# Performance work log

Measured on AMD Instinct MI355X. Metric: run time of the kernel, lower is better.

## Reference

```python
import jax, jax.numpy as jnp
import numpy as np

EMBED_DIM = 1024
NUM_HEADS = 16
HEAD_DIM = EMBED_DIM // NUM_HEADS
SCALE = float(np.sqrt(HEAD_DIM))


def setup_inputs() -> dict:
    key = jax.random.key(0)
    ks = jax.random.split(key, 7)
    B, S, E = 2, 2048, EMBED_DIM
    query = jax.random.normal(ks[0], (B, S, E), dtype=jnp.float32)
    key_t = jax.random.normal(ks[1], (B, S, E), dtype=jnp.float32)
    value = jax.random.normal(ks[2], (B, S, E), dtype=jnp.float32)
    # nn.Linear(E, E, bias=False): weight shape (out, in); y = x @ W.T
    std = 1.0 / np.sqrt(E)
    Wq = jax.random.uniform(ks[3], (E, E), jnp.float32, -std, std)
    Wk = jax.random.uniform(ks[4], (E, E), jnp.float32, -std, std)
    Wv = jax.random.uniform(ks[5], (E, E), jnp.float32, -std, std)
    Wo = jax.random.uniform(ks[6], (E, E), jnp.float32, -std, std)
    return {"query": query, "key": key_t, "value": value,
            "Wq": Wq, "Wk": Wk, "Wv": Wv, "Wo": Wo}


def reference(query, key, value, Wq, Wk, Wv, Wo):
    B, S, E = query.shape
    H, D = NUM_HEADS, HEAD_DIM
    q = (query @ Wq.T).reshape(B, S, H, D).transpose(0, 2, 1, 3)  # [B,H,S,D]
    k = (key @ Wk.T).reshape(B, S, H, D).transpose(0, 2, 1, 3)
    v = (value @ Wv.T).reshape(B, S, H, D).transpose(0, 2, 1, 3)
    scores = jnp.einsum('bhqd,bhkd->bhqk', q, k) / SCALE  # [B,H,S,S]
    attn = jax.nn.softmax(scores, axis=-1)
    out = jnp.einsum('bhqk,bhkd->bhqd', attn, v)  # [B,H,S,D]
    out = out.transpose(0, 2, 1, 3).reshape(B, S, E)
    return out @ Wo.T
```

## Files before the change

kernel.cpp:

```cpp
#include <hip/hip_runtime.h>
#include <hip/hip_bf16.h>
#include <math.h>

typedef float f32x4 __attribute__((ext_vector_type(4)));
typedef __bf16 bf16x8 __attribute__((ext_vector_type(8)));
typedef unsigned short u16;
typedef u16 u16x8 __attribute__((ext_vector_type(8)));
typedef u16 u16x4 __attribute__((ext_vector_type(4)));

__device__ __forceinline__ u16 f2bf(float f) {
    unsigned u = __builtin_bit_cast(unsigned, f);
    u = (u + 0x7fffu + ((u >> 16) & 1u)) >> 16;
    return (u16)u;
}
__device__ __forceinline__ unsigned pack2_rhu(float a, float b) {
    return __builtin_amdgcn_perm(__builtin_bit_cast(unsigned, b) + 0x8000u,
                                 __builtin_bit_cast(unsigned, a) + 0x8000u,
                                 0x07060302u);
}

#if __has_builtin(__builtin_amdgcn_exp2f)
#define EXP2(x) __builtin_amdgcn_exp2f(x)
#else
#define EXP2(x) exp2f(x)
#endif

__device__ __forceinline__ void gload16(const u16* g, u16* l) {
    __builtin_amdgcn_global_load_lds(
        (const __attribute__((address_space(1))) unsigned int*)(g),
        (__attribute__((address_space(3))) unsigned int*)(l), 16, 0, 0);
}

__global__ __launch_bounds__(256) void cast_all(
    const float* __restrict__ q, const float* __restrict__ k, const float* __restrict__ v,
    const float* __restrict__ wq, const float* __restrict__ wk, const float* __restrict__ wv,
    const float* __restrict__ wo, u16* __restrict__ dst) {
    int i = blockIdx.x * 256 + threadIdx.x;
    const float* src;
    int off;
    if (i < 3145728) {
        int seg = i >> 20;
        src = (seg == 0) ? q : (seg == 1) ? k : v;
        off = i - (seg << 20);
    } else {
        int j = (i - 3145728) >> 18;
        src = (j == 0) ? wq : (j == 1) ? wk : (j == 2) ? wv : wo;
        off = (i - 3145728) - (j << 18);
    }
    float4 val = ((const float4*)src)[off];
    u16x4 o4;
    o4.x = f2bf(val.x); o4.y = f2bf(val.y); o4.z = f2bf(val.z); o4.w = f2bf(val.w);
    ((u16x4*)dst)[i] = o4;
}

__global__ __launch_bounds__(256) void qkv_gemm(
    const u16* __restrict__ Xq, const u16* __restrict__ Xk, const u16* __restrict__ Xv,
    const u16* __restrict__ Wq, const u16* __restrict__ Wk, const u16* __restrict__ Wv,
    u16* __restrict__ Qo, u16* __restrict__ Ko, u16* __restrict__ Vto) {
    constexpr int K = 1024;
    const int z = blockIdx.z;
    const u16* __restrict__ A = (z == 0) ? Xq : (z == 1) ? Xk : Xv;
    const u16* __restrict__ W = (z == 0) ? Wq : (z == 1) ? Wk : Wv;
    u16* __restrict__ Out = (z == 0) ? Qo : (z == 1) ? Ko : Vto;

    __shared__ __align__(16) u16 As[128 * 64];
    __shared__ __align__(16) u16 Bs[128 * 64];

    const int t = threadIdx.x;
    const int lane = t & 63, wave = t >> 6;
    const int quad = lane >> 4, c = lane & 15, cx = c & 7;
    const int wr = (wave >> 1) * 64, wc = (wave & 1) * 64;
    const int rowA0 = blockIdx.y * 128;
    const int colB0 = blockIdx.x * 128;

    const int l3 = lane >> 3, l7 = lane & 7;
    const int chs = (l7 ^ l3) << 3;
    const u16* gA[4];
    const u16* gB[4];
    u16* lA[4];
    u16* lB[4];
#pragma unroll
    for (int i = 0; i < 4; ++i) {
        int row = wave * 32 + i * 8 + l3;
        gA[i] = A + (size_t)(rowA0 + row) * K + chs;
        gB[i] = W + (size_t)(colB0 + row) * K + chs;
        lA[i] = As + (wave * 256 + i * 64) * 8;
        lB[i] = Bs + (wave * 256 + i * 64) * 8;
    }

    const f32x4 zero4 = {0.f, 0.f, 0.f, 0.f};
    f32x4 acc[4][4];
#pragma unroll
    for (int i = 0; i < 4; ++i)
#pragma unroll
        for (int j = 0; j < 4; ++j) acc[i][j] = zero4;

    for (int kt = 0; kt < K; kt += 64) {
        __syncthreads();
#pragma unroll
        for (int i = 0; i < 4; ++i) {
            gload16(gA[i] + kt, lA[i]);
            gload16(gB[i] + kt, lB[i]);
        }
        __syncthreads();
#pragma unroll
        for (int ks = 0; ks < 2; ++ks) {
            const int co = ((ks * 4 + quad) ^ cx) << 3;
            bf16x8 af[4], bfr[4];
#pragma unroll
            for (int i = 0; i < 4; ++i)
                af[i] = *(const bf16x8*)(As + (wr + i * 16 + c) * 64 + co);
#pragma unroll
            for (int j = 0; j < 4; ++j)
                bfr[j] = *(const bf16x8*)(Bs + (wc + j * 16 + c) * 64 + co);
            if (z == 2) {
#pragma unroll
                for (int i = 0; i < 4; ++i)
#pragma unroll
                    for (int j = 0; j < 4; ++j)
                        acc[i][j] = __builtin_amdgcn_mfma_f32_16x16x32_bf16(bfr[j], af[i], acc[i][j], 0, 0, 0);
            } else {
#pragma unroll
                for (int i = 0; i < 4; ++i)
#pragma unroll
                    for (int j = 0; j < 4; ++j)
                        acc[i][j] = __builtin_amdgcn_mfma_f32_16x16x32_bf16(af[i], bfr[j], acc[i][j], 0, 0, 0);
            }
        }
    }

    const float scale = (z == 0) ? 0.18033688011112042f : 1.0f;
#pragma unroll
    for (int i = 0; i < 4; ++i) {
#pragma unroll
        for (int j = 0; j < 4; ++j) {
#pragma unroll
            for (int r = 0; r < 4; ++r) {
                float v = acc[i][j][r];
                if (z == 2) {
                    int n = colB0 + wc + j * 16 + quad * 4 + r;
                    int m = rowA0 + wr + i * 16 + c;
                    int b = m >> 11, s = m & 2047, h = n >> 6, d = n & 63;
                    Out[((((b << 4) | h) << 6) + d) * 2048 + s] = f2bf(v);
                } else {
                    int m = rowA0 + wr + i * 16 + quad * 4 + r;
                    int n = colB0 + wc + j * 16 + c;
                    int b = m >> 11, s = m & 2047, h = n >> 6, d = n & 63;
                    Out[((((b << 4) | h) * 2048 + s) << 6) + d] = f2bf(v * scale);
                }
            }
        }
    }
}

__global__ __launch_bounds__(256, 2) void out_gemm(const u16* __restrict__ A,
                                                   const u16* __restrict__ W,
                                                   float* __restrict__ Out) {
    constexpr int K = 1024;
    __shared__ __align__(16) u16 As[64 * 64];
    __shared__ __align__(16) u16 Bs[128 * 64];
    const int t = threadIdx.x;
    const int lane = t & 63, wave = t >> 6;
    const int quad = lane >> 4, c = lane & 15, cx = c & 7;
    const int wr = (wave >> 1) * 32, wc = (wave & 1) * 64;
    const int rowA0 = blockIdx.y * 64;
    const int colB0 = blockIdx.x * 128;

    const int l3 = lane >> 3, l7 = lane & 7;
    const int chs = (l7 ^ l3) << 3;
    const u16* gA[2];
    const u16* gB[4];
    u16* lA[2];
    u16* lB[4];
#pragma unroll
    for (int i = 0; i < 2; ++i) {
        int row = wave * 16 + i * 8 + l3;
        gA[i] = A + (size_t)(rowA0 + row) * K + chs;
        lA[i] = As + (wave * 128 + i * 64) * 8;
    }
#pragma unroll
    for (int i = 0; i < 4; ++i) {
        int row = wave * 32 + i * 8 + l3;
        gB[i] = W + (size_t)(colB0 + row) * K + chs;
        lB[i] = Bs + (wave * 256 + i * 64) * 8;
    }

    const f32x4 zero4 = {0.f, 0.f, 0.f, 0.f};
    f32x4 acc[2][4];
#pragma unroll
    for (int i = 0; i < 2; ++i)
#pragma unroll
        for (int j = 0; j < 4; ++j) acc[i][j] = zero4;

    for (int kt = 0; kt < K; kt += 64) {
        __syncthreads();
#pragma unroll
        for (int i = 0; i < 2; ++i) gload16(gA[i] + kt, lA[i]);
#pragma unroll
        for (int i = 0; i < 4; ++i) gload16(gB[i] + kt, lB[i]);
        __syncthreads();
#pragma unroll
        for (int ks = 0; ks < 2; ++ks) {
            const int co = ((ks * 4 + quad) ^ cx) << 3;
            bf16x8 af[2], bfr[4];
#pragma unroll
            for (int i = 0; i < 2; ++i)
                af[i] = *(const bf16x8*)(As + (wr + i * 16 + c) * 64 + co);
#pragma unroll
            for (int j = 0; j < 4; ++j)
                bfr[j] = *(const bf16x8*)(Bs + (wc + j * 16 + c) * 64 + co);
#pragma unroll
            for (int i = 0; i < 2; ++i)
#pragma unroll
                for (int j = 0; j < 4; ++j)
                    acc[i][j] = __builtin_amdgcn_mfma_f32_16x16x32_bf16(af[i], bfr[j], acc[i][j], 0, 0, 0);
        }
    }
#pragma unroll
    for (int i = 0; i < 2; ++i)
#pragma unroll
        for (int j = 0; j < 4; ++j)
#pragma unroll
            for (int r = 0; r < 4; ++r) {
                int m = rowA0 + wr + i * 16 + quad * 4 + r;
                int n = colB0 + wc + j * 16 + c;
                Out[(m << 10) + n] = acc[i][j][r];
            }
}

__global__ __launch_bounds__(256, 2) void flash_attn(const u16* __restrict__ Qp,
                                                     const u16* __restrict__ Kp,
                                                     const u16* __restrict__ Vt,
                                                     u16* __restrict__ Ob) {
    constexpr int S = 2048;
    const int bh = blockIdx.y;
    const int b = bh >> 4, h = bh & 15;
    const int t = threadIdx.x, wave = t >> 6, lane = t & 63;
    const int quad = lane >> 4, c = lane & 15, cx = c & 7;
    const int qw = blockIdx.x * 128 + wave * 32;
    const u16* Qb = Qp + (bh * S + qw) * 64;
    const u16* Kb = Kp + (bh * S) * 64;
    const u16* Vb = Vt + bh * 64 * S;

    __shared__ __align__(16) u16 Ks[2][64 * 64];
    __shared__ __align__(16) u16 Vs[2][64 * 64];
    __shared__ __align__(16) u16 Ps[4][32 * 64];
    u16* Pw = &Ps[wave][0];

    bf16x8 qf[2][2];
#pragma unroll
    for (int qt = 0; qt < 2; ++qt)
#pragma unroll
        for (int hf = 0; hf < 2; ++hf)
            qf[qt][hf] = *(const bf16x8*)(Qb + (qt * 16 + c) * 64 + hf * 32 + quad * 8);

    const int l3 = lane >> 3, l7 = lane & 7;
    const int chs = (l7 ^ l3) << 3;
    const u16* gK[2];
    const u16* gV[2];
    int lbase[2];
#pragma unroll
    for (int i = 0; i < 2; ++i) {
        int row = wave * 16 + i * 8 + l3;
        gK[i] = Kb + row * 64 + chs;
        gV[i] = Vb + row * 2048 + chs;
        lbase[i] = (wave * 128 + i * 64) * 8;
    }
#pragma unroll
    for (int i = 0; i < 2; ++i) {
        gload16(gK[i], &Ks[0][lbase[i]]);
        gload16(gV[i], &Vs[0][lbase[i]]);
    }
    __syncthreads();

    const f32x4 zero4 = {0.f, 0.f, 0.f, 0.f};
    f32x4 o[2][4];
#pragma unroll
    for (int qt = 0; qt < 2; ++qt)
#pragma unroll
        for (int t2 = 0; t2 < 4; ++t2) o[qt][t2] = zero4;
    float lsum[2] = {0.f, 0.f};

    for (int it = 0; it < S / 64; ++it) {
        const int cur = it & 1;
        if (it + 1 < S / 64) {
#pragma unroll
            for (int i = 0; i < 2; ++i) {
                gload16(gK[i] + (it + 1) * 4096, &Ks[cur ^ 1][lbase[i]]);
                gload16(gV[i] + (it + 1) * 64, &Vs[cur ^ 1][lbase[i]]);
            }
        }
        const u16* Kc = &Ks[cur][0];
        const u16* Vc = &Vs[cur][0];
        const int co0 = (quad ^ cx) << 3, co1 = ((4 + quad) ^ cx) << 3;
        f32x4 sc[4][2];
#pragma unroll
        for (int kt = 0; kt < 4; ++kt) {
            const int krow = (kt * 16 + c) * 64;
            bf16x8 kf0 = *(const bf16x8*)(Kc + krow + co0);
            bf16x8 kf1 = *(const bf16x8*)(Kc + krow + co1);
#pragma unroll
            for (int qt = 0; qt < 2; ++qt) {
                f32x4 zz = zero4;
                zz = __builtin_amdgcn_mfma_f32_16x16x32_bf16(kf0, qf[qt][0], zz, 0, 0, 0);
                zz = __builtin_amdgcn_mfma_f32_16x16x32_bf16(kf1, qf[qt][1], zz, 0, 0, 0);
                sc[kt][qt] = zz;
            }
        }
#pragma unroll
        for (int kt = 0; kt < 4; ++kt) {
            const int pchunk = ((kt * 2 + (quad >> 1)) ^ cx) << 3;
#pragma unroll
            for (int qt = 0; qt < 2; ++qt) {
                float p0 = EXP2(sc[kt][qt][0]);
                float p1 = EXP2(sc[kt][qt][1]);
                float p2 = EXP2(sc[kt][qt][2]);
                float p3 = EXP2(sc[kt][qt][3]);
                lsum[qt] += (p0 + p1) + (p2 + p3);
                uint2 pk;
                pk.x = pack2_rhu(p0, p1);
                pk.y = pack2_rhu(p2, p3);
                *(uint2*)(Pw + (qt * 16 + c) * 64 + pchunk + (quad & 1) * 4) = pk;
            }
        }
        __asm__ __volatile__("s_waitcnt lgkmcnt(0)" ::: "memory");
        bf16x8 pf[2][2];
#pragma unroll
        for (int qt = 0; qt < 2; ++qt) {
            pf[qt][0] = *(const bf16x8*)(Pw + (qt * 16 + c) * 64 + co0);
            pf[qt][1] = *(const bf16x8*)(Pw + (qt * 16 + c) * 64 + co1);
        }
#pragma unroll
        for (int t2 = 0; t2 < 4; ++t2) {
            const int vrow = (t2 * 16 + c) * 64;
            bf16x8 vf0 = *(const bf16x8*)(Vc + vrow + co0);
            bf16x8 vf1 = *(const bf16x8*)(Vc + vrow + co1);
#pragma unroll
            for (int qt = 0; qt < 2; ++qt) {
                o[qt][t2] = __builtin_amdgcn_mfma_f32_16x16x32_bf16(pf[qt][0], vf0, o[qt][t2], 0, 0, 0);
                o[qt][t2] = __builtin_amdgcn_mfma_f32_16x16x32_bf16(pf[qt][1], vf1, o[qt][t2], 0, 0, 0);
            }
        }
        __syncthreads();
    }
#pragma unroll
    for (int qt = 0; qt < 2; ++qt) {
        lsum[qt] += __shfl_xor(lsum[qt], 16);
        lsum[qt] += __shfl_xor(lsum[qt], 32);
    }
#pragma unroll
    for (int qt = 0; qt < 2; ++qt)
#pragma unroll
        for (int r = 0; r < 4; ++r) {
            float inv = 1.f / __shfl(lsum[qt], quad * 4 + r);
            int row = qw + qt * 16 + quad * 4 + r;
            int base = ((b * S + row) * 16 + h) * 64;
#pragma unroll
            for (int t2 = 0; t2 < 4; ++t2)
                Ob[base + t2 * 16 + c] = f2bf(o[qt][t2][r] * inv);
        }
}

extern "C" void kernel_launch(void* const* d_in, const int* in_sizes, int n_in,
                              void* d_out, int out_size, void* d_ws, size_t ws_size,
                              hipStream_t stream) {
    const float* q  = (const float*)d_in[0];
    const float* k  = (const float*)d_in[1];
    const float* v  = (const float*)d_in[2];
    const float* wq = (const float*)d_in[3];
    const float* wk = (const float*)d_in[4];
    const float* wv = (const float*)d_in[5];
    const float* wo = (const float*)d_in[6];

    u16* ws = (u16*)d_ws;
    u16* qb  = ws;
    u16* kb  = ws + 4194304;
    u16* vb  = ws + 8388608;
    u16* wqb = ws + 12582912;
    u16* wkb = ws + 13631488;
    u16* wvb = ws + 14680064;
    u16* wob = ws + 15728640;
    u16* Qp  = ws + 16777216;
    u16* Kp  = ws + 20971520;
    u16* Vtp = ws + 25165824;
    u16* Obf = ws + 29360128;

    cast_all<<<16384, 256, 0, stream>>>(q, k, v, wq, wk, wv, wo, ws);

    qkv_gemm<<<dim3(8, 32, 3), 256, 0, stream>>>(qb, kb, vb, wqb, wkb, wvb, Qp, Kp, Vtp);

    flash_attn<<<dim3(16, 32), 256, 0, stream>>>(Qp, Kp, Vtp, Obf);

    out_gemm<<<dim3(8, 64), 256, 0, stream>>>(Obf, wob, (float*)d_out);
}
```

Before: 221.5 us.

## Remap block indices for XCD-aware L2 locality and compute row sums via MFMA

Flattens the grids of all three GEMM and attention kernels into 1D and remaps block indices. The aim is for blocks that share weights, or the same batch-head K/V, to land on the same XCD under round-robin dispatch and so reuse its L2. In flash_attn it also drops the per-lane scalar softmax row-sum and the final shuffles. The row sum is now accumulated with an extra MFMA against a vector of bf16 ones, which moves VALU adds onto the matrix unit but sums the bf16-rounded probabilities rather than the fp32 ones.

```diff
diff --git a/kernel.cpp b/kernel.cpp
--- a/kernel.cpp
+++ b/kernel.cpp
@@ -58,7 +58,11 @@
     const u16* __restrict__ Wq, const u16* __restrict__ Wk, const u16* __restrict__ Wv,
     u16* __restrict__ Qo, u16* __restrict__ Ko, u16* __restrict__ Vto) {
     constexpr int K = 1024;
-    const int z = blockIdx.z;
+    const int blk = blockIdx.x;
+    const int xb = blk / 96;
+    const int zb = (blk % 96) >> 5;
+    const int yb = blk & 31;
+    const int z = zb;
     const u16* __restrict__ A = (z == 0) ? Xq : (z == 1) ? Xk : Xv;
     const u16* __restrict__ W = (z == 0) ? Wq : (z == 1) ? Wk : Wv;
     u16* __restrict__ Out = (z == 0) ? Qo : (z == 1) ? Ko : Vto;
@@ -70,8 +74,8 @@
     const int lane = t & 63, wave = t >> 6;
     const int quad = lane >> 4, c = lane & 15, cx = c & 7;
     const int wr = (wave >> 1) * 64, wc = (wave & 1) * 64;
-    const int rowA0 = blockIdx.y * 128;
-    const int colB0 = blockIdx.x * 128;
+    const int rowA0 = yb * 128;
+    const int colB0 = xb * 128;
 
     const int l3 = lane >> 3, l7 = lane & 7;
     const int chs = (l7 ^ l3) << 3;
@@ -159,12 +163,15 @@
     constexpr int K = 1024;
     __shared__ __align__(16) u16 As[64 * 64];
     __shared__ __align__(16) u16 Bs[128 * 64];
+    const int blk = blockIdx.x;
+    const int yb = blk & 63;
+    const int xb = blk >> 6;
     const int t = threadIdx.x;
     const int lane = t & 63, wave = t >> 6;
     const int quad = lane >> 4, c = lane & 15, cx = c & 7;
     const int wr = (wave >> 1) * 32, wc = (wave & 1) * 64;
-    const int rowA0 = blockIdx.y * 64;
-    const int colB0 = blockIdx.x * 128;
+    const int rowA0 = yb * 64;
+    const int colB0 = xb * 128;
 
     const int l3 = lane >> 3, l7 = lane & 7;
     const int chs = (l7 ^ l3) << 3;
@@ -233,11 +240,13 @@
                                                      const u16* __restrict__ Vt,
                                                      u16* __restrict__ Ob) {
     constexpr int S = 2048;
-    const int bh = blockIdx.y;
+    const int blk = blockIdx.x;
+    const int j = blk & 31;
+    const int bh = ((j & 7) << 2) | (j >> 3);
     const int b = bh >> 4, h = bh & 15;
     const int t = threadIdx.x, wave = t >> 6, lane = t & 63;
     const int quad = lane >> 4, c = lane & 15, cx = c & 7;
-    const int qw = blockIdx.x * 128 + wave * 32;
+    const int qw = (blk >> 5) * 128 + wave * 32;
     const u16* Qb = Qp + (bh * S + qw) * 64;
     const u16* Kb = Kp + (bh * S) * 64;
     const u16* Vb = Vt + bh * 64 * S;
@@ -253,6 +262,11 @@
 #pragma unroll
         for (int hf = 0; hf < 2; ++hf)
             qf[qt][hf] = *(const bf16x8*)(Qb + (qt * 16 + c) * 64 + hf * 32 + quad * 8);
+
+    u16x8 ou;
+#pragma unroll
+    for (int i = 0; i < 8; ++i) ou[i] = 0x3F80;
+    const bf16x8 onesf = __builtin_bit_cast(bf16x8, ou);
 
     const int l3 = lane >> 3, l7 = lane & 7;
     const int chs = (l7 ^ l3) << 3;
@@ -275,11 +289,15 @@
 
     const f32x4 zero4 = {0.f, 0.f, 0.f, 0.f};
     f32x4 o[2][4];
-#pragma unroll
-    for (int qt = 0; qt < 2; ++qt)
+    f32x4 ol[2];
+#pragma unroll
+    for (int qt = 0; qt < 2; ++qt) {
+        ol[qt] = zero4;
 #pragma unroll
         for (int t2 = 0; t2 < 4; ++t2) o[qt][t2] = zero4;
-    float lsum[2] = {0.f, 0.f};
+    }
+
+    const int co0 = (quad ^ cx) << 3, co1 = ((4 + quad) ^ cx) << 3;
 
     for (int it = 0; it < S / 64; ++it) {
         const int cur = it & 1;
@@ -292,7 +310,6 @@
         }
         const u16* Kc = &Ks[cur][0];
         const u16* Vc = &Vs[cur][0];
-        const int co0 = (quad ^ cx) << 3, co1 = ((4 + quad) ^ cx) << 3;
         f32x4 sc[4][2];
 #pragma unroll
         for (int kt = 0; kt < 4; ++kt) {
@@ -316,7 +333,6 @@
                 float p1 = EXP2(sc[kt][qt][1]);
                 float p2 = EXP2(sc[kt][qt][2]);
                 float p3 = EXP2(sc[kt][qt][3]);
-                lsum[qt] += (p0 + p1) + (p2 + p3);
                 uint2 pk;
                 pk.x = pack2_rhu(p0, p1);
                 pk.y = pack2_rhu(p2, p3);
@@ -331,6 +347,11 @@
             pf[qt][1] = *(const bf16x8*)(Pw + (qt * 16 + c) * 64 + co1);
         }
 #pragma unroll
+        for (int qt = 0; qt < 2; ++qt) {
+            ol[qt] = __builtin_amdgcn_mfma_f32_16x16x32_bf16(pf[qt][0], onesf, ol[qt], 0, 0, 0);
+            ol[qt] = __builtin_amdgcn_mfma_f32_16x16x32_bf16(pf[qt][1], onesf, ol[qt], 0, 0, 0);
+        }
+#pragma unroll
         for (int t2 = 0; t2 < 4; ++t2) {
             const int vrow = (t2 * 16 + c) * 64;
             bf16x8 vf0 = *(const bf16x8*)(Vc + vrow + co0);
@@ -344,15 +365,10 @@
         __syncthreads();
     }
 #pragma unroll
-    for (int qt = 0; qt < 2; ++qt) {
-        lsum[qt] += __shfl_xor(lsum[qt], 16);
-        lsum[qt] += __shfl_xor(lsum[qt], 32);
-    }
-#pragma unroll
     for (int qt = 0; qt < 2; ++qt)
 #pragma unroll
         for (int r = 0; r < 4; ++r) {
-            float inv = 1.f / __shfl(lsum[qt], quad * 4 + r);
+            float inv = 1.f / ol[qt][r];
             int row = qw + qt * 16 + quad * 4 + r;
             int base = ((b * S + row) * 16 + h) * 64;
 #pragma unroll
@@ -387,9 +403,9 @@
 
     cast_all<<<16384, 256, 0, stream>>>(q, k, v, wq, wk, wv, wo, ws);
 
-    qkv_gemm<<<dim3(8, 32, 3), 256, 0, stream>>>(qb, kb, vb, wqb, wkb, wvb, Qp, Kp, Vtp);
-
-    flash_attn<<<dim3(16, 32), 256, 0, stream>>>(Qp, Kp, Vtp, Obf);
-
-    out_gemm<<<dim3(8, 64), 256, 0, stream>>>(Obf, wob, (float*)d_out);
-}
+    qkv_gemm<<<768, 256, 0, stream>>>(qb, kb, vb, wqb, wkb, wvb, Qp, Kp, Vtp);
+
+    flash_attn<<<512, 256, 0, stream>>>(Qp, Kp, Vtp, Obf);
+
+    out_gemm<<<512, 256, 0, stream>>>(Obf, wob, (float*)d_out);
+}
```

New measurement: 214.2 us. 3.3% less time.
